# Kernel optimization log

Hardware: AMD Instinct MI355X
Metric: run time of the kernel (lower is better)

Reference implementation:

```python
import jax, jax.numpy as jnp
import numpy as np

N = 100000
E = 1600000
F_IN = 16
HEADS = 4
OUT_CH = 32  # conv_filters[i] // heads = 128 // 4
HID = HEADS * OUT_CH  # 128
N_GRAPHS = 64
N_TARGETS = 4
EPS_BN = 1e-5


def setup_inputs() -> dict:
    key = jax.random.key(0)
    ks = jax.random.split(key, 32)
    glorot = lambda k, shp: jax.random.normal(k, shp, jnp.float32) * np.sqrt(2.0 / (shp[0] + shp[-1]))
    inp = {
        "node_features": jax.random.normal(ks[0], (N, F_IN), jnp.float32),
        "edge_index": jax.random.randint(ks[1], (2, E), 0, N, jnp.int64),
        "batch": jnp.sort(jax.random.randint(ks[2], (N,), 0, N_GRAPHS, jnp.int64)),
        # GAT layer 1: F_IN -> HEADS*OUT_CH
        "W1": glorot(ks[3], (F_IN, HID)),
        "b1": jnp.zeros((HID,), jnp.float32),
        "att_src1": glorot(ks[4], (HEADS, OUT_CH)),
        "att_dst1": glorot(ks[5], (HEADS, OUT_CH)),
        "bn_g1": jnp.ones((HID,), jnp.float32),
        "bn_b1": jnp.zeros((HID,), jnp.float32),
        # GAT layer 2: HID -> HID
        "W2": glorot(ks[6], (HID, HID)),
        "b2": jnp.zeros((HID,), jnp.float32),
        "att_src2": glorot(ks[7], (HEADS, OUT_CH)),
        "att_dst2": glorot(ks[8], (HEADS, OUT_CH)),
        "bn_g2": jnp.ones((HID,), jnp.float32),
        "bn_b2": jnp.zeros((HID,), jnp.float32),
        # dense head 128 -> 64 -> 32 -> 4
        "d1_W": glorot(ks[9], (HID, HID // 2)),
        "d1_b": jnp.zeros((HID // 2,), jnp.float32),
        "bn_g_d1": jnp.ones((HID // 2,), jnp.float32),
        "bn_b_d1": jnp.zeros((HID // 2,), jnp.float32),
        "d2_W": glorot(ks[10], (HID // 2, HID // 4)),
        "d2_b": jnp.zeros((HID // 4,), jnp.float32),
        "bn_g_d2": jnp.ones((HID // 4,), jnp.float32),
        "bn_b_d2": jnp.zeros((HID // 4,), jnp.float32),
        "fc_W": glorot(ks[11], (HID // 4, N_TARGETS)),
        "fc_b": jnp.zeros((N_TARGETS,), jnp.float32),
    }
    return inp


def batch_norm(x, gamma, beta):
    # training-mode BatchNorm1d: biased batch stats over dim 0
    mu = jnp.mean(x, axis=0)
    var = jnp.mean(jnp.square(x - mu), axis=0)
    return gamma * (x - mu) * jax.lax.rsqrt(var + EPS_BN) + beta


def gat_conv(x, src, dst, W, b, att_src, att_dst):
    # PyG GATConv (shared lin, concat heads): h = x @ W -> [N, H, C]
    h = (x @ W).reshape(-1, HEADS, OUT_CH)
    a_s = jnp.sum(h * att_src, axis=-1)  # [N, H]
    a_d = jnp.sum(h * att_dst, axis=-1)  # [N, H]
    e = jax.nn.leaky_relu(a_s[src] + a_d[dst], 0.2)  # [E, H]
    # softmax over incoming edges per destination node
    m = jax.ops.segment_max(e, dst, num_segments=N)
    m = jnp.where(jnp.isfinite(m), m, 0.0)
    w = jnp.exp(e - m[dst])
    s = jax.ops.segment_sum(w, dst, num_segments=N)
    alpha = w / (s[dst] + 1e-16)  # [E, H]
    out = jax.ops.segment_sum(h[src] * alpha[:, :, None], dst, num_segments=N)
    return out.reshape(-1, HID) + b


def reference(node_features, edge_index, batch,
              W1, b1, att_src1, att_dst1, bn_g1, bn_b1,
              W2, b2, att_src2, att_dst2, bn_g2, bn_b2,
              d1_W, d1_b, bn_g_d1, bn_b_d1,
              d2_W, d2_b, bn_g_d2, bn_b_d2,
              fc_W, fc_b):
    src, dst = edge_index[0], edge_index[1]
    x = gat_conv(node_features, src, dst, W1, b1, att_src1, att_dst1)
    x = jax.nn.relu(batch_norm(x, bn_g1, bn_b1))
    x = gat_conv(x, src, dst, W2, b2, att_src2, att_dst2)
    x = jax.nn.relu(batch_norm(x, bn_g2, bn_b2))
    # global mean pool over graphs
    sums = jax.ops.segment_sum(x, batch, num_segments=N_GRAPHS)
    cnt = jax.ops.segment_sum(jnp.ones((x.shape[0],), x.dtype), batch, num_segments=N_GRAPHS)
    g = sums / jnp.maximum(cnt, 1.0)[:, None]  # [G, HID]
    g = jax.nn.relu(batch_norm(g @ d1_W + d1_b, bn_g_d1, bn_b_d1))
    g = jax.nn.relu(batch_norm(g @ d2_W + d2_b, bn_g_d2, bn_b_d2))
    return g @ fc_W + fc_b
```

## Files before the change

kernel.cpp:

```cpp
#include <hip/hip_runtime.h>

#define HID 128
#define NG 64

__device__ __forceinline__ float lrelu(float v) { return v > 0.0f ? v : 0.2f * v; }

__device__ __forceinline__ unsigned int bf16rne(float f) {
    unsigned int u = __float_as_uint(f);
    return (u + 0x7fffu + ((u >> 16) & 1u)) >> 16;
}
__device__ __forceinline__ unsigned int packbf(float a, float b) {
    return bf16rne(a) | (bf16rne(b) << 16);
}

template <int K, bool BN>
__global__ __launch_bounds__(256) void k_gemm(const float* __restrict__ xin,
        const float* __restrict__ W,
        const float* __restrict__ scale, const float* __restrict__ shift,
        const float* __restrict__ attS, const float* __restrict__ attD,
        unsigned short* __restrict__ h, float* __restrict__ as_, float* __restrict__ ad_, int N)
{
    __shared__ float xs[64][K];
    constexpr int K4 = K / 4;
    int t = threadIdx.x;
    int cq = t & 31;
    int nr = t >> 5;

    float4 atS = ((const float4*)attS)[cq];
    float4 atD = ((const float4*)attD)[cq];

    for (int n0 = blockIdx.x * 64; n0 < N; n0 += gridDim.x * 64) {
        int nrem = N - n0; if (nrem > 64) nrem = 64;
        for (int idx = t; idx < 64 * K4; idx += 256) {
            int n = idx / K4, k4 = idx % K4;
            float4 v = make_float4(0.f, 0.f, 0.f, 0.f);
            if (n < nrem) {
                v = ((const float4*)(xin + (size_t)(n0 + n) * K))[k4];
                if (BN) {
                    float4 sc = ((const float4*)scale)[k4];
                    float4 sh = ((const float4*)shift)[k4];
                    v.x = fmaf(v.x, sc.x, sh.x); v.x = v.x > 0.f ? v.x : 0.f;
                    v.y = fmaf(v.y, sc.y, sh.y); v.y = v.y > 0.f ? v.y : 0.f;
                    v.z = fmaf(v.z, sc.z, sh.z); v.z = v.z > 0.f ? v.z : 0.f;
                    v.w = fmaf(v.w, sc.w, sh.w); v.w = v.w > 0.f ? v.w : 0.f;
                }
            }
            *(float4*)(&xs[n][k4 * 4]) = v;
        }
        __syncthreads();

        float4 acc[8];
#pragma unroll
        for (int j = 0; j < 8; ++j) acc[j] = make_float4(0.f, 0.f, 0.f, 0.f);

        const float4* W4 = (const float4*)W;
#pragma unroll 2
        for (int k4 = 0; k4 < K4; ++k4) {
            float4 w0 = W4[(k4 * 4 + 0) * 32 + cq];
            float4 w1 = W4[(k4 * 4 + 1) * 32 + cq];
            float4 w2 = W4[(k4 * 4 + 2) * 32 + cq];
            float4 w3 = W4[(k4 * 4 + 3) * 32 + cq];
#pragma unroll
            for (int j = 0; j < 8; ++j) {
                float4 xv = *(const float4*)(&xs[nr * 8 + j][k4 * 4]);
                acc[j].x = fmaf(xv.x, w0.x, acc[j].x);
                acc[j].y = fmaf(xv.x, w0.y, acc[j].y);
                acc[j].z = fmaf(xv.x, w0.z, acc[j].z);
                acc[j].w = fmaf(xv.x, w0.w, acc[j].w);
                acc[j].x = fmaf(xv.y, w1.x, acc[j].x);
                acc[j].y = fmaf(xv.y, w1.y, acc[j].y);
                acc[j].z = fmaf(xv.y, w1.z, acc[j].z);
                acc[j].w = fmaf(xv.y, w1.w, acc[j].w);
                acc[j].x = fmaf(xv.z, w2.x, acc[j].x);
                acc[j].y = fmaf(xv.z, w2.y, acc[j].y);
                acc[j].z = fmaf(xv.z, w2.z, acc[j].z);
                acc[j].w = fmaf(xv.z, w2.w, acc[j].w);
                acc[j].x = fmaf(xv.w, w3.x, acc[j].x);
                acc[j].y = fmaf(xv.w, w3.y, acc[j].y);
                acc[j].z = fmaf(xv.w, w3.z, acc[j].z);
                acc[j].w = fmaf(xv.w, w3.w, acc[j].w);
            }
        }

#pragma unroll
        for (int j = 0; j < 8; ++j) {
            int n = nr * 8 + j;
            bool ok = (n < nrem);
            if (ok) {
                unsigned int lo = packbf(acc[j].x, acc[j].y);
                unsigned int hi = packbf(acc[j].z, acc[j].w);
                ((uint2*)(h + (size_t)(n0 + n) * 128))[cq] = make_uint2(lo, hi);
            }
            float ps = acc[j].x * atS.x + acc[j].y * atS.y + acc[j].z * atS.z + acc[j].w * atS.w;
            float pd = acc[j].x * atD.x + acc[j].y * atD.y + acc[j].z * atD.z + acc[j].w * atD.w;
            ps += __shfl_xor(ps, 1); pd += __shfl_xor(pd, 1);
            ps += __shfl_xor(ps, 2); pd += __shfl_xor(pd, 2);
            ps += __shfl_xor(ps, 4); pd += __shfl_xor(pd, 4);
            if (ok && (cq & 7) == 0) {
                int hd = cq >> 3;
                as_[(size_t)(n0 + n) * 4 + hd] = ps;
                ad_[(size_t)(n0 + n) * 4 + hd] = pd;
            }
        }
        __syncthreads();
    }
}

__global__ __launch_bounds__(256) void k_bhist(const int* __restrict__ ei,
        int* __restrict__ bSize, int E, int nB)
{
    __shared__ int hist[1024];
    int t = threadIdx.x;
    for (int i = t; i < nB; i += 256) hist[i] = 0;
    __syncthreads();
    int chunk = (E + gridDim.x - 1) / gridDim.x;
    int lo = blockIdx.x * chunk, hi = lo + chunk; if (hi > E) hi = E;
    for (int e = lo + t; e < hi; e += 256) atomicAdd(&hist[ei[E + e] >> 8], 1);
    __syncthreads();
    for (int i = t; i < nB; i += 256) { int c = hist[i]; if (c) atomicAdd(&bSize[i], c); }
}

__global__ __launch_bounds__(512) void k_bscan(const int* __restrict__ bSize,
        int* __restrict__ bOff, int* __restrict__ bCur, int nB)
{
    __shared__ int part[512];
    int t = threadIdx.x;
    part[t] = (t < nB) ? bSize[t] : 0;
    __syncthreads();
    for (int off = 1; off < 512; off <<= 1) {
        int u = (t >= off) ? part[t - off] : 0;
        __syncthreads();
        part[t] += u;
        __syncthreads();
    }
    int ex = (t == 0) ? 0 : part[t - 1];
    if (t < nB) { bOff[t] = ex; bCur[t] = ex; }
    if (t == nB - 1) bOff[nB] = part[t];
}

__global__ __launch_bounds__(256) void k_part(const int* __restrict__ ei,
        int* __restrict__ bCur, unsigned int* __restrict__ bucketBuf, int E, int nB)
{
    __shared__ int hist[1024];
    __shared__ int base[1024];
    int t = threadIdx.x;
    int chunk = (E + gridDim.x - 1) / gridDim.x;
    int lo = blockIdx.x * chunk, hi = lo + chunk; if (hi > E) hi = E;
    for (int i = t; i < nB; i += 256) hist[i] = 0;
    __syncthreads();
    for (int e = lo + t; e < hi; e += 256) atomicAdd(&hist[ei[E + e] >> 8], 1);
    __syncthreads();
    for (int i = t; i < nB; i += 256) {
        int c = hist[i];
        base[i] = c ? atomicAdd(&bCur[i], c) : 0;
        hist[i] = 0;
    }
    __syncthreads();
    for (int e = lo + t; e < hi; e += 256) {
        int s = ei[e], d = ei[E + e];
        int b = d >> 8;
        int pos = base[b] + atomicAdd(&hist[b], 1);
        bucketBuf[pos] = ((unsigned)(d & 255) << 24) | (unsigned)s;
    }
}

__global__ __launch_bounds__(256) void k_build(const unsigned int* __restrict__ bucketBuf,
        const int* __restrict__ bOff, int* __restrict__ rowPtr, int* __restrict__ sSrc, int N)
{
    __shared__ int lhist[256];
    __shared__ int sOut[8192];
    int b = blockIdx.x;
    int dlo = b << 8;
    int dhi = dlo + 256; if (dhi > N) dhi = N;
    int base = bOff[b], end = bOff[b + 1];
    int sz = end - base;
    int t = threadIdx.x;
    lhist[t] = 0;
    __syncthreads();
    for (int i = t; i < sz; i += 256) {
        atomicAdd(&lhist[bucketBuf[base + i] >> 24], 1);
    }
    __syncthreads();
    for (int off = 1; off < 256; off <<= 1) {
        int u = (t >= off) ? lhist[t - off] : 0;
        __syncthreads();
        lhist[t] += u;
        __syncthreads();
    }
    int pfx = (t == 0) ? 0 : lhist[t - 1];
    if (dlo + t < dhi) rowPtr[dlo + t] = base + pfx;
    if (t == 0 && dhi == N) rowPtr[N] = end;
    __syncthreads();
    lhist[t] = pfx;
    __syncthreads();
    if (sz <= 8192) {
        for (int i = t; i < sz; i += 256) {
            unsigned int p = bucketBuf[base + i];
            int pos = atomicAdd(&lhist[p >> 24], 1);
            sOut[pos] = (int)(p & 0xffffffu);
        }
        __syncthreads();
        for (int i = t; i < sz; i += 256) sSrc[base + i] = sOut[i];
    } else {
        for (int i = t; i < sz; i += 256) {
            unsigned int p = bucketBuf[base + i];
            int pos = atomicAdd(&lhist[p >> 24], 1);
            sSrc[base + pos] = (int)(p & 0xffffffu);
        }
    }
}

__global__ __launch_bounds__(256) void k_agg(const int* __restrict__ rowPtr,
        const int* __restrict__ sSrc,
        const float* __restrict__ as_, const float* __restrict__ ad_,
        const unsigned short* __restrict__ h, float* __restrict__ out, int N)
{
    int t = threadIdx.x;
    int lane = t & 31;
    int d = blockIdx.x * 8 + (t >> 5);
    if (d >= N) return;
    int hd = lane >> 3;
    int b0 = rowPtr[d], b1 = rowPtr[d + 1];
    float4 adv = ((const float4*)ad_)[d];

    float4 sm = make_float4(0.f, 0.f, 0.f, 0.f);
    for (int j = b0 + lane; j < b1; j += 32) {
        int s = sSrc[j];
        float4 a = ((const float4*)as_)[s];
        sm.x += __expf(lrelu(a.x + adv.x));
        sm.y += __expf(lrelu(a.y + adv.y));
        sm.z += __expf(lrelu(a.z + adv.z));
        sm.w += __expf(lrelu(a.w + adv.w));
    }
#pragma unroll
    for (int off = 1; off < 32; off <<= 1) {
        sm.x += __shfl_xor(sm.x, off);
        sm.y += __shfl_xor(sm.y, off);
        sm.z += __shfl_xor(sm.z, off);
        sm.w += __shfl_xor(sm.w, off);
    }
    float sumh = (hd == 0) ? sm.x : (hd == 1) ? sm.y : (hd == 2) ? sm.z : sm.w;
    float inv = 1.f / (sumh + 1e-16f);
    float advh = (hd == 0) ? adv.x : (hd == 1) ? adv.y : (hd == 2) ? adv.z : adv.w;

    const uint2* h2 = (const uint2*)h;
    float4 acc = make_float4(0.f, 0.f, 0.f, 0.f);
    int j = b0;
    for (; j + 4 <= b1; j += 4) {
        int s0 = sSrc[j], s1 = sSrc[j + 1], s2 = sSrc[j + 2], s3 = sSrc[j + 3];
        float w0 = __expf(lrelu(as_[(size_t)s0 * 4 + hd] + advh));
        float w1 = __expf(lrelu(as_[(size_t)s1 * 4 + hd] + advh));
        float w2 = __expf(lrelu(as_[(size_t)s2 * 4 + hd] + advh));
        float w3 = __expf(lrelu(as_[(size_t)s3 * 4 + hd] + advh));
        uint2 u0 = h2[(size_t)s0 * 32 + lane];
        uint2 u1 = h2[(size_t)s1 * 32 + lane];
        uint2 u2 = h2[(size_t)s2 * 32 + lane];
        uint2 u3 = h2[(size_t)s3 * 32 + lane];
        acc.x = fmaf(w0, __uint_as_float(u0.x << 16), acc.x);
        acc.y = fmaf(w0, __uint_as_float(u0.x & 0xffff0000u), acc.y);
        acc.z = fmaf(w0, __uint_as_float(u0.y << 16), acc.z);
        acc.w = fmaf(w0, __uint_as_float(u0.y & 0xffff0000u), acc.w);
        acc.x = fmaf(w1, __uint_as_float(u1.x << 16), acc.x);
        acc.y = fmaf(w1, __uint_as_float(u1.x & 0xffff0000u), acc.y);
        acc.z = fmaf(w1, __uint_as_float(u1.y << 16), acc.z);
        acc.w = fmaf(w1, __uint_as_float(u1.y & 0xffff0000u), acc.w);
        acc.x = fmaf(w2, __uint_as_float(u2.x << 16), acc.x);
        acc.y = fmaf(w2, __uint_as_float(u2.x & 0xffff0000u), acc.y);
        acc.z = fmaf(w2, __uint_as_float(u2.y << 16), acc.z);
        acc.w = fmaf(w2, __uint_as_float(u2.y & 0xffff0000u), acc.w);
        acc.x = fmaf(w3, __uint_as_float(u3.x << 16), acc.x);
        acc.y = fmaf(w3, __uint_as_float(u3.x & 0xffff0000u), acc.y);
        acc.z = fmaf(w3, __uint_as_float(u3.y << 16), acc.z);
        acc.w = fmaf(w3, __uint_as_float(u3.y & 0xffff0000u), acc.w);
    }
    for (; j < b1; ++j) {
        int s = sSrc[j];
        float w = __expf(lrelu(as_[(size_t)s * 4 + hd] + advh));
        uint2 u = h2[(size_t)s * 32 + lane];
        acc.x = fmaf(w, __uint_as_float(u.x << 16), acc.x);
        acc.y = fmaf(w, __uint_as_float(u.x & 0xffff0000u), acc.y);
        acc.z = fmaf(w, __uint_as_float(u.y << 16), acc.z);
        acc.w = fmaf(w, __uint_as_float(u.y & 0xffff0000u), acc.w);
    }
    acc.x *= inv; acc.y *= inv; acc.z *= inv; acc.w *= inv;
    ((float4*)out)[(size_t)d * 32 + lane] = acc;
}

__global__ __launch_bounds__(256) void k_bnstats(const float* __restrict__ x,
        double* __restrict__ sums, int N)
{
    __shared__ float r1[256], r2[256];
    int t = threadIdx.x;
    int c = t & 127;
    int half = t >> 7;
    float s1 = 0.f, s2 = 0.f;
    for (int n = blockIdx.x * 2 + half; n < N; n += gridDim.x * 2) {
        float v = x[(size_t)n * 128 + c];
        s1 += v; s2 += v * v;
    }
    r1[t] = s1; r2[t] = s2;
    __syncthreads();
    if (t < 128) {
        s1 = r1[t] + r1[t + 128];
        s2 = r2[t] + r2[t + 128];
        atomicAdd(&sums[t], (double)s1);
        atomicAdd(&sums[128 + t], (double)s2);
    }
}

__global__ __launch_bounds__(128) void k_bnscale(const double* __restrict__ sums,
        const float* __restrict__ gamma, const float* __restrict__ beta,
        float* __restrict__ scale, float* __restrict__ shift, int N)
{
    int c = threadIdx.x;
    double mu = sums[c] / (double)N;
    double var = sums[128 + c] / (double)N - mu * mu;
    if (var < 0.0) var = 0.0;
    double rs = 1.0 / sqrt(var + 1e-5);
    float sc = (float)((double)gamma[c] * rs);
    scale[c] = sc;
    shift[c] = beta[c] - (float)mu * sc;
}

__global__ __launch_bounds__(128) void k_pool(const float* __restrict__ x,
        const int* __restrict__ batch, const float* __restrict__ scale, const float* __restrict__ shift,
        float* __restrict__ gsum, float* __restrict__ gcnt, int N)
{
    int lane = threadIdx.x & 31;
    int r = threadIdx.x >> 5;
    int n0 = blockIdx.x * 64;
    if (n0 >= N) return;
    int n1 = n0 + 64; if (n1 > N) n1 = N;
    float4 sc = ((const float4*)scale)[lane];
    float4 sh = ((const float4*)shift)[lane];
    float4 acc = make_float4(0.f, 0.f, 0.f, 0.f);
    int cnt = 0, cur = -1;
    for (int n = n0 + r; n < n1; n += 4) {
        int g = batch[n];
        if (g != cur) {
            if (cur >= 0) {
                atomicAdd(&gsum[cur * 128 + lane * 4 + 0], acc.x);
                atomicAdd(&gsum[cur * 128 + lane * 4 + 1], acc.y);
                atomicAdd(&gsum[cur * 128 + lane * 4 + 2], acc.z);
                atomicAdd(&gsum[cur * 128 + lane * 4 + 3], acc.w);
                if (lane == 0) atomicAdd(&gcnt[cur], (float)cnt);
            }
            acc = make_float4(0.f, 0.f, 0.f, 0.f); cnt = 0; cur = g;
        }
        float4 v = ((const float4*)x)[(size_t)n * 32 + lane];
        v.x = fmaf(v.x, sc.x, sh.x); v.x = v.x > 0.f ? v.x : 0.f;
        v.y = fmaf(v.y, sc.y, sh.y); v.y = v.y > 0.f ? v.y : 0.f;
        v.z = fmaf(v.z, sc.z, sh.z); v.z = v.z > 0.f ? v.z : 0.f;
        v.w = fmaf(v.w, sc.w, sh.w); v.w = v.w > 0.f ? v.w : 0.f;
        acc.x += v.x; acc.y += v.y; acc.z += v.z; acc.w += v.w;
        cnt++;
    }
    if (cur >= 0) {
        atomicAdd(&gsum[cur * 128 + lane * 4 + 0], acc.x);
        atomicAdd(&gsum[cur * 128 + lane * 4 + 1], acc.y);
        atomicAdd(&gsum[cur * 128 + lane * 4 + 2], acc.z);
        atomicAdd(&gsum[cur * 128 + lane * 4 + 3], acc.w);
        if (lane == 0) atomicAdd(&gcnt[cur], (float)cnt);
    }
}

__global__ __launch_bounds__(256) void k_head(const float* __restrict__ gsum, const float* __restrict__ gcnt,
        const float* __restrict__ d1W, const float* __restrict__ d1b,
        const float* __restrict__ g_d1, const float* __restrict__ b_d1,
        const float* __restrict__ d2W, const float* __restrict__ d2b,
        const float* __restrict__ g_d2, const float* __restrict__ b_d2,
        const float* __restrict__ fcW, const float* __restrict__ fcb,
        float* __restrict__ out)
{
    __shared__ float G[64 * 128];
    __shared__ float Y1[64 * 64];
    __shared__ float Y2[64 * 32];
    int t = threadIdx.x;
    for (int i = t; i < 64 * 128; i += 256) {
        int g = i >> 7;
        float cv = gcnt[g]; if (cv < 1.f) cv = 1.f;
        G[i] = gsum[i] / cv;
    }
    __syncthreads();
    for (int i = t; i < 64 * 64; i += 256) {
        int r = i >> 6, j = i & 63;
        float a = 0.f;
        for (int k = 0; k < 128; ++k) a = fmaf(G[r * 128 + k], d1W[k * 64 + j], a);
        Y1[i] = a + d1b[j];
    }
    __syncthreads();
    if (t < 64) {
        float s1 = 0.f, s2 = 0.f;
        for (int r = 0; r < 64; ++r) { float v = Y1[r * 64 + t]; s1 += v; s2 += v * v; }
        float mu = s1 / 64.f, var = s2 / 64.f - mu * mu; if (var < 0.f) var = 0.f;
        float rs = 1.0f / sqrtf(var + 1e-5f);
        float scv = g_d1[t] * rs, shv = b_d1[t] - mu * scv;
        for (int r = 0; r < 64; ++r) {
            float v = fmaf(Y1[r * 64 + t], scv, shv);
            Y1[r * 64 + t] = v > 0.f ? v : 0.f;
        }
    }
    __syncthreads();
    for (int i = t; i < 64 * 32; i += 256) {
        int r = i >> 5, j = i & 31;
        float a = 0.f;
        for (int k = 0; k < 64; ++k) a = fmaf(Y1[r * 64 + k], d2W[k * 32 + j], a);
        Y2[i] = a + d2b[j];
    }
    __syncthreads();
    if (t < 32) {
        float s1 = 0.f, s2 = 0.f;
        for (int r = 0; r < 64; ++r) { float v = Y2[r * 32 + t]; s1 += v; s2 += v * v; }
        float mu = s1 / 64.f, var = s2 / 64.f - mu * mu; if (var < 0.f) var = 0.f;
        float rs = 1.0f / sqrtf(var + 1e-5f);
        float scv = g_d2[t] * rs, shv = b_d2[t] - mu * scv;
        for (int r = 0; r < 64; ++r) {
            float v = fmaf(Y2[r * 32 + t], scv, shv);
            Y2[r * 32 + t] = v > 0.f ? v : 0.f;
        }
    }
    __syncthreads();
    {
        int r = t >> 2, j = t & 3;
        float a = 0.f;
        for (int k = 0; k < 32; ++k) a = fmaf(Y2[r * 32 + k], fcW[k * 4 + j], a);
        out[t] = a + fcb[j];
    }
}

extern "C" void kernel_launch(void* const* d_in, const int* in_sizes, int n_in,
                              void* d_out, int out_size, void* d_ws, size_t ws_size,
                              hipStream_t stream) {
    const int N = in_sizes[0] / 16;
    const int E = in_sizes[1] / 2;
    const int nB = (N + 255) >> 8;

    const float* x        = (const float*)d_in[0];
    const int*   ei       = (const int*)d_in[1];
    const int*   batch    = (const int*)d_in[2];
    const float* W1       = (const float*)d_in[3];
    const float* att_s1   = (const float*)d_in[5];
    const float* att_d1   = (const float*)d_in[6];
    const float* bn_g1    = (const float*)d_in[7];
    const float* bn_b1    = (const float*)d_in[8];
    const float* W2       = (const float*)d_in[9];
    const float* att_s2   = (const float*)d_in[11];
    const float* att_d2   = (const float*)d_in[12];
    const float* bn_g2    = (const float*)d_in[13];
    const float* bn_b2    = (const float*)d_in[14];
    const float* d1W      = (const float*)d_in[15];
    const float* d1b      = (const float*)d_in[16];
    const float* g_d1     = (const float*)d_in[17];
    const float* b_d1     = (const float*)d_in[18];
    const float* d2W      = (const float*)d_in[19];
    const float* d2b      = (const float*)d_in[20];
    const float* g_d2     = (const float*)d_in[21];
    const float* b_d2     = (const float*)d_in[22];
    const float* fcW      = (const float*)d_in[23];
    const float* fcb      = (const float*)d_in[24];
    float* out = (float*)d_out;

    float* ws = (float*)d_ws;
    size_t o = 0;
    unsigned short* hbuf = (unsigned short*)(ws + o); o += (size_t)N * 64;
    float* outb   = ws + o;  o += (size_t)N * 128;
    float* as_    = ws + o;  o += (size_t)N * 4;
    float* ad_    = ws + o;  o += (size_t)N * 4;
    float* scale1 = ws + o;  o += 128;
    float* shift1 = ws + o;  o += 128;
    float* scale2 = ws + o;  o += 128;
    float* shift2 = ws + o;  o += 128;
    size_t zoff = o;
    double* bnsumA = (double*)(ws + o); o += 512;
    double* bnsumB = (double*)(ws + o); o += 512;
    float* gsum   = ws + o;  o += 64 * 128;
    float* gcnt   = ws + o;  o += 64;
    int*   bSize  = (int*)(ws + o); o += 1024;
    size_t zbytes = (o - zoff) * 4;
    int* rowPtr   = (int*)(ws + o); o += (size_t)N + 1;
    int* sSrc     = (int*)(ws + o); o += E;
    int* bOff     = (int*)(ws + o); o += 1025;
    int* bCur     = (int*)(ws + o); o += 1024;
    unsigned int* bucketBuf = (unsigned int*)(ws + o); o += E;

    hipMemsetAsync(ws + zoff, 0, zbytes, stream);

    k_bhist<<<256, 256, 0, stream>>>(ei, bSize, E, nB);
    k_bscan<<<1, 512, 0, stream>>>(bSize, bOff, bCur, nB);
    k_part<<<256, 256, 0, stream>>>(ei, bCur, bucketBuf, E, nB);
    k_build<<<nB, 256, 0, stream>>>(bucketBuf, bOff, rowPtr, sSrc, N);

    int gemm_grid = (N + 63) / 64;
    int agg_grid = (N + 7) / 8;

    k_gemm<16, false><<<gemm_grid, 256, 0, stream>>>(x, W1, nullptr, nullptr,
            att_s1, att_d1, hbuf, as_, ad_, N);
    k_agg<<<agg_grid, 256, 0, stream>>>(rowPtr, sSrc, as_, ad_, hbuf, outb, N);
    k_bnstats<<<1024, 256, 0, stream>>>(outb, bnsumA, N);
    k_bnscale<<<1, 128, 0, stream>>>(bnsumA, bn_g1, bn_b1, scale1, shift1, N);

    k_gemm<128, true><<<gemm_grid, 256, 0, stream>>>(outb, W2, scale1, shift1,
            att_s2, att_d2, hbuf, as_, ad_, N);
    k_agg<<<agg_grid, 256, 0, stream>>>(rowPtr, sSrc, as_, ad_, hbuf, outb, N);
    k_bnstats<<<1024, 256, 0, stream>>>(outb, bnsumB, N);
    k_bnscale<<<1, 128, 0, stream>>>(bnsumB, bn_g2, bn_b2, scale2, shift2, N);

    k_pool<<<(N + 63) / 64, 128, 0, stream>>>(outb, batch, scale2, shift2, gsum, gcnt, N);
    k_head<<<1, 256, 0, stream>>>(gsum, gcnt, d1W, d1b, g_d1, b_d1,
                                  d2W, d2b, g_d2, b_d2, fcW, fcb, out);
}
```

Measured before the change: 540.8 us.

## Cache attention weights in LDS, fuse BN scale into consumers, vectorize bnstats

The aggregation kernel now stores the per-edge exp attention weights computed in the softmax-sum pass in shared memory (up to 64 edges per node), so the accumulation pass reuses them instead of reloading as_ and recomputing exp. That loop is unrolled by 8 to keep more gathers in flight. The separate BN scale/shift kernels are removed; each gemm and pool block recomputes scale and shift from the double sums into LDS, saving two launches at the cost of redundant per-block work. bnstats is vectorized with float4 loads and runs on fewer blocks.

```diff
diff --git a/kernel.cpp b/kernel.cpp
--- a/kernel.cpp
+++ b/kernel.cpp
@@ -16,15 +16,30 @@
 template <int K, bool BN>
 __global__ __launch_bounds__(256) void k_gemm(const float* __restrict__ xin,
         const float* __restrict__ W,
-        const float* __restrict__ scale, const float* __restrict__ shift,
+        const double* __restrict__ bnsum, const float* __restrict__ gamma, const float* __restrict__ beta,
         const float* __restrict__ attS, const float* __restrict__ attD,
         unsigned short* __restrict__ h, float* __restrict__ as_, float* __restrict__ ad_, int N)
 {
     __shared__ float xs[64][K];
+    __shared__ __align__(16) float sc_s[K];
+    __shared__ __align__(16) float sh_s[K];
     constexpr int K4 = K / 4;
     int t = threadIdx.x;
     int cq = t & 31;
     int nr = t >> 5;
+
+    if (BN) {
+        if (t < K) {
+            double mu = bnsum[t] / (double)N;
+            double var = bnsum[K + t] / (double)N - mu * mu;
+            if (var < 0.0) var = 0.0;
+            double rs = 1.0 / sqrt(var + 1e-5);
+            float sc = (float)((double)gamma[t] * rs);
+            sc_s[t] = sc;
+            sh_s[t] = beta[t] - (float)mu * sc;
+        }
+        __syncthreads();
+    }
 
     float4 atS = ((const float4*)attS)[cq];
     float4 atD = ((const float4*)attD)[cq];
@@ -37,8 +52,8 @@
             if (n < nrem) {
                 v = ((const float4*)(xin + (size_t)(n0 + n) * K))[k4];
                 if (BN) {
-                    float4 sc = ((const float4*)scale)[k4];
-                    float4 sh = ((const float4*)shift)[k4];
+                    float4 sc = ((const float4*)sc_s)[k4];
+                    float4 sh = ((const float4*)sh_s)[k4];
                     v.x = fmaf(v.x, sc.x, sh.x); v.x = v.x > 0.f ? v.x : 0.f;
                     v.y = fmaf(v.y, sc.y, sh.y); v.y = v.y > 0.f ? v.y : 0.f;
                     v.z = fmaf(v.z, sc.z, sh.z); v.z = v.z > 0.f ? v.z : 0.f;
@@ -215,22 +230,27 @@
         const float* __restrict__ as_, const float* __restrict__ ad_,
         const unsigned short* __restrict__ h, float* __restrict__ out, int N)
 {
+    __shared__ float wst[8][64][4];
     int t = threadIdx.x;
     int lane = t & 31;
-    int d = blockIdx.x * 8 + (t >> 5);
-    if (d >= N) return;
-    int hd = lane >> 3;
-    int b0 = rowPtr[d], b1 = rowPtr[d + 1];
-    float4 adv = ((const float4*)ad_)[d];
+    int g = t >> 5;
+    int d = blockIdx.x * 8 + g;
+    bool valid = (d < N);
+    int b0 = 0, deg = 0;
+    float4 adv = make_float4(0.f, 0.f, 0.f, 0.f);
+    if (valid) { b0 = rowPtr[d]; deg = rowPtr[d + 1] - b0; adv = ((const float4*)ad_)[d]; }
 
     float4 sm = make_float4(0.f, 0.f, 0.f, 0.f);
-    for (int j = b0 + lane; j < b1; j += 32) {
-        int s = sSrc[j];
+    for (int e = lane; e < deg; e += 32) {
+        int s = sSrc[b0 + e];
         float4 a = ((const float4*)as_)[s];
-        sm.x += __expf(lrelu(a.x + adv.x));
-        sm.y += __expf(lrelu(a.y + adv.y));
-        sm.z += __expf(lrelu(a.z + adv.z));
-        sm.w += __expf(lrelu(a.w + adv.w));
+        float4 w;
+        w.x = __expf(lrelu(a.x + adv.x));
+        w.y = __expf(lrelu(a.y + adv.y));
+        w.z = __expf(lrelu(a.z + adv.z));
+        w.w = __expf(lrelu(a.w + adv.w));
+        if (e < 64) *(float4*)(&wst[g][e][0]) = w;
+        sm.x += w.x; sm.y += w.y; sm.z += w.z; sm.w += w.w;
     }
 #pragma unroll
     for (int off = 1; off < 32; off <<= 1) {
@@ -239,23 +259,32 @@
         sm.z += __shfl_xor(sm.z, off);
         sm.w += __shfl_xor(sm.w, off);
     }
+    __syncthreads();
+
+    int hd = lane >> 3;
     float sumh = (hd == 0) ? sm.x : (hd == 1) ? sm.y : (hd == 2) ? sm.z : sm.w;
+    float advh = (hd == 0) ? adv.x : (hd == 1) ? adv.y : (hd == 2) ? adv.z : adv.w;
     float inv = 1.f / (sumh + 1e-16f);
-    float advh = (hd == 0) ? adv.x : (hd == 1) ? adv.y : (hd == 2) ? adv.z : adv.w;
 
     const uint2* h2 = (const uint2*)h;
+    const int* sp = sSrc + b0;
     float4 acc = make_float4(0.f, 0.f, 0.f, 0.f);
-    int j = b0;
-    for (; j + 4 <= b1; j += 4) {
-        int s0 = sSrc[j], s1 = sSrc[j + 1], s2 = sSrc[j + 2], s3 = sSrc[j + 3];
-        float w0 = __expf(lrelu(as_[(size_t)s0 * 4 + hd] + advh));
-        float w1 = __expf(lrelu(as_[(size_t)s1 * 4 + hd] + advh));
-        float w2 = __expf(lrelu(as_[(size_t)s2 * 4 + hd] + advh));
-        float w3 = __expf(lrelu(as_[(size_t)s3 * 4 + hd] + advh));
-        uint2 u0 = h2[(size_t)s0 * 32 + lane];
-        uint2 u1 = h2[(size_t)s1 * 32 + lane];
-        uint2 u2 = h2[(size_t)s2 * 32 + lane];
-        uint2 u3 = h2[(size_t)s3 * 32 + lane];
+    int dc = deg < 64 ? deg : 64;
+    int j = 0;
+#define AGG1(S, W) { uint2 u = h2[(size_t)(S) * 32 + lane]; \
+        acc.x = fmaf((W), __uint_as_float(u.x << 16), acc.x); \
+        acc.y = fmaf((W), __uint_as_float(u.x & 0xffff0000u), acc.y); \
+        acc.z = fmaf((W), __uint_as_float(u.y << 16), acc.z); \
+        acc.w = fmaf((W), __uint_as_float(u.y & 0xffff0000u), acc.w); }
+    for (; j + 8 <= dc; j += 8) {
+        int s0 = sp[j], s1 = sp[j+1], s2 = sp[j+2], s3 = sp[j+3];
+        int s4 = sp[j+4], s5 = sp[j+5], s6 = sp[j+6], s7 = sp[j+7];
+        float w0 = wst[g][j][hd],   w1 = wst[g][j+1][hd], w2 = wst[g][j+2][hd], w3 = wst[g][j+3][hd];
+        float w4 = wst[g][j+4][hd], w5 = wst[g][j+5][hd], w6 = wst[g][j+6][hd], w7 = wst[g][j+7][hd];
+        uint2 u0 = h2[(size_t)s0*32+lane], u1 = h2[(size_t)s1*32+lane];
+        uint2 u2 = h2[(size_t)s2*32+lane], u3 = h2[(size_t)s3*32+lane];
+        uint2 u4 = h2[(size_t)s4*32+lane], u5 = h2[(size_t)s5*32+lane];
+        uint2 u6 = h2[(size_t)s6*32+lane], u7 = h2[(size_t)s7*32+lane];
         acc.x = fmaf(w0, __uint_as_float(u0.x << 16), acc.x);
         acc.y = fmaf(w0, __uint_as_float(u0.x & 0xffff0000u), acc.y);
         acc.z = fmaf(w0, __uint_as_float(u0.y << 16), acc.z);
@@ -272,67 +301,100 @@
         acc.y = fmaf(w3, __uint_as_float(u3.x & 0xffff0000u), acc.y);
         acc.z = fmaf(w3, __uint_as_float(u3.y << 16), acc.z);
         acc.w = fmaf(w3, __uint_as_float(u3.y & 0xffff0000u), acc.w);
-    }
-    for (; j < b1; ++j) {
-        int s = sSrc[j];
+        acc.x = fmaf(w4, __uint_as_float(u4.x << 16), acc.x);
+        acc.y = fmaf(w4, __uint_as_float(u4.x & 0xffff0000u), acc.y);
+        acc.z = fmaf(w4, __uint_as_float(u4.y << 16), acc.z);
+        acc.w = fmaf(w4, __uint_as_float(u4.y & 0xffff0000u), acc.w);
+        acc.x = fmaf(w5, __uint_as_float(u5.x << 16), acc.x);
+        acc.y = fmaf(w5, __uint_as_float(u5.x & 0xffff0000u), acc.y);
+        acc.z = fmaf(w5, __uint_as_float(u5.y << 16), acc.z);
+        acc.w = fmaf(w5, __uint_as_float(u5.y & 0xffff0000u), acc.w);
+        acc.x = fmaf(w6, __uint_as_float(u6.x << 16), acc.x);
+        acc.y = fmaf(w6, __uint_as_float(u6.x & 0xffff0000u), acc.y);
+        acc.z = fmaf(w6, __uint_as_float(u6.y << 16), acc.z);
+        acc.w = fmaf(w6, __uint_as_float(u6.y & 0xffff0000u), acc.w);
+        acc.x = fmaf(w7, __uint_as_float(u7.x << 16), acc.x);
+        acc.y = fmaf(w7, __uint_as_float(u7.x & 0xffff0000u), acc.y);
+        acc.z = fmaf(w7, __uint_as_float(u7.y << 16), acc.z);
+        acc.w = fmaf(w7, __uint_as_float(u7.y & 0xffff0000u), acc.w);
+    }
+    for (; j < dc; ++j) {
+        float w = wst[g][j][hd];
+        AGG1(sp[j], w);
+    }
+    for (; j < deg; ++j) {
+        int s = sp[j];
         float w = __expf(lrelu(as_[(size_t)s * 4 + hd] + advh));
-        uint2 u = h2[(size_t)s * 32 + lane];
-        acc.x = fmaf(w, __uint_as_float(u.x << 16), acc.x);
-        acc.y = fmaf(w, __uint_as_float(u.x & 0xffff0000u), acc.y);
-        acc.z = fmaf(w, __uint_as_float(u.y << 16), acc.z);
-        acc.w = fmaf(w, __uint_as_float(u.y & 0xffff0000u), acc.w);
-    }
-    acc.x *= inv; acc.y *= inv; acc.z *= inv; acc.w *= inv;
-    ((float4*)out)[(size_t)d * 32 + lane] = acc;
+        AGG1(s, w);
+    }
+#undef AGG1
+    if (valid) {
+        acc.x *= inv; acc.y *= inv; acc.z *= inv; acc.w *= inv;
+        ((float4*)out)[(size_t)d * 32 + lane] = acc;
+    }
 }
 
 __global__ __launch_bounds__(256) void k_bnstats(const float* __restrict__ x,
         double* __restrict__ sums, int N)
 {
-    __shared__ float r1[256], r2[256];
-    int t = threadIdx.x;
-    int c = t & 127;
-    int half = t >> 7;
-    float s1 = 0.f, s2 = 0.f;
-    for (int n = blockIdx.x * 2 + half; n < N; n += gridDim.x * 2) {
-        float v = x[(size_t)n * 128 + c];
-        s1 += v; s2 += v * v;
+    __shared__ float4 r1[256], r2[256];
+    int t = threadIdx.x;
+    int lane = t & 31;
+    int rg = t >> 5;
+    const float4* x4 = (const float4*)x;
+    float4 s1 = make_float4(0.f, 0.f, 0.f, 0.f);
+    float4 s2 = make_float4(0.f, 0.f, 0.f, 0.f);
+    for (int n = blockIdx.x * 8 + rg; n < N; n += gridDim.x * 8) {
+        float4 v = x4[(size_t)n * 32 + lane];
+        s1.x += v.x; s1.y += v.y; s1.z += v.z; s1.w += v.w;
+        s2.x += v.x * v.x; s2.y += v.y * v.y; s2.z += v.z * v.z; s2.w += v.w * v.w;
     }
     r1[t] = s1; r2[t] = s2;
     __syncthreads();
-    if (t < 128) {
-        s1 = r1[t] + r1[t + 128];
-        s2 = r2[t] + r2[t + 128];
-        atomicAdd(&sums[t], (double)s1);
-        atomicAdd(&sums[128 + t], (double)s2);
-    }
-}
-
-__global__ __launch_bounds__(128) void k_bnscale(const double* __restrict__ sums,
-        const float* __restrict__ gamma, const float* __restrict__ beta,
-        float* __restrict__ scale, float* __restrict__ shift, int N)
-{
-    int c = threadIdx.x;
-    double mu = sums[c] / (double)N;
-    double var = sums[128 + c] / (double)N - mu * mu;
-    if (var < 0.0) var = 0.0;
-    double rs = 1.0 / sqrt(var + 1e-5);
-    float sc = (float)((double)gamma[c] * rs);
-    scale[c] = sc;
-    shift[c] = beta[c] - (float)mu * sc;
+    if (t < 32) {
+        float4 a = r1[t], b = r2[t];
+        for (int k = 1; k < 8; ++k) {
+            float4 c = r1[t + 32 * k], e = r2[t + 32 * k];
+            a.x += c.x; a.y += c.y; a.z += c.z; a.w += c.w;
+            b.x += e.x; b.y += e.y; b.z += e.z; b.w += e.w;
+        }
+        atomicAdd(&sums[t * 4 + 0], (double)a.x);
+        atomicAdd(&sums[t * 4 + 1], (double)a.y);
+        atomicAdd(&sums[t * 4 + 2], (double)a.z);
+        atomicAdd(&sums[t * 4 + 3], (double)a.w);
+        atomicAdd(&sums[128 + t * 4 + 0], (double)b.x);
+        atomicAdd(&sums[128 + t * 4 + 1], (double)b.y);
+        atomicAdd(&sums[128 + t * 4 + 2], (double)b.z);
+        atomicAdd(&sums[128 + t * 4 + 3], (double)b.w);
+    }
 }
 
 __global__ __launch_bounds__(128) void k_pool(const float* __restrict__ x,
-        const int* __restrict__ batch, const float* __restrict__ scale, const float* __restrict__ shift,
+        const int* __restrict__ batch,
+        const double* __restrict__ bnsum, const float* __restrict__ gamma, const float* __restrict__ beta,
         float* __restrict__ gsum, float* __restrict__ gcnt, int N)
 {
-    int lane = threadIdx.x & 31;
-    int r = threadIdx.x >> 5;
+    __shared__ __align__(16) float sc_s[128];
+    __shared__ __align__(16) float sh_s[128];
+    int t = threadIdx.x;
+    {
+        double mu = bnsum[t] / (double)N;
+        double var = bnsum[128 + t] / (double)N - mu * mu;
+        if (var < 0.0) var = 0.0;
+        double rs = 1.0 / sqrt(var + 1e-5);
+        float sc = (float)((double)gamma[t] * rs);
+        sc_s[t] = sc;
+        sh_s[t] = beta[t] - (float)mu * sc;
+    }
+    __syncthreads();
+
+    int lane = t & 31;
+    int r = t >> 5;
     int n0 = blockIdx.x * 64;
     if (n0 >= N) return;
     int n1 = n0 + 64; if (n1 > N) n1 = N;
-    float4 sc = ((const float4*)scale)[lane];
-    float4 sh = ((const float4*)shift)[lane];
+    float4 sc = ((const float4*)sc_s)[lane];
+    float4 sh = ((const float4*)sh_s)[lane];
     float4 acc = make_float4(0.f, 0.f, 0.f, 0.f);
     int cnt = 0, cur = -1;
     for (int n = n0 + r; n < n1; n += 4) {
@@ -466,10 +528,6 @@
     float* outb   = ws + o;  o += (size_t)N * 128;
     float* as_    = ws + o;  o += (size_t)N * 4;
     float* ad_    = ws + o;  o += (size_t)N * 4;
-    float* scale1 = ws + o;  o += 128;
-    float* shift1 = ws + o;  o += 128;
-    float* scale2 = ws + o;  o += 128;
-    float* shift2 = ws + o;  o += 128;
     size_t zoff = o;
     double* bnsumA = (double*)(ws + o); o += 512;
     double* bnsumB = (double*)(ws + o); o += 512;
@@ -493,19 +551,17 @@
     int gemm_grid = (N + 63) / 64;
     int agg_grid = (N + 7) / 8;
 
-    k_gemm<16, false><<<gemm_grid, 256, 0, stream>>>(x, W1, nullptr, nullptr,
+    k_gemm<16, false><<<gemm_grid, 256, 0, stream>>>(x, W1, nullptr, nullptr, nullptr,
             att_s1, att_d1, hbuf, as_, ad_, N);
     k_agg<<<agg_grid, 256, 0, stream>>>(rowPtr, sSrc, as_, ad_, hbuf, outb, N);
-    k_bnstats<<<1024, 256, 0, stream>>>(outb, bnsumA, N);
-    k_bnscale<<<1, 128, 0, stream>>>(bnsumA, bn_g1, bn_b1, scale1, shift1, N);
-
-    k_gemm<128, true><<<gemm_grid, 256, 0, stream>>>(outb, W2, scale1, shift1,
+    k_bnstats<<<512, 256, 0, stream>>>(outb, bnsumA, N);
+
+    k_gemm<128, true><<<gemm_grid, 256, 0, stream>>>(outb, W2, bnsumA, bn_g1, bn_b1,
             att_s2, att_d2, hbuf, as_, ad_, N);
     k_agg<<<agg_grid, 256, 0, stream>>>(rowPtr, sSrc, as_, ad_, hbuf, outb, N);
-    k_bnstats<<<1024, 256, 0, stream>>>(outb, bnsumB, N);
-    k_bnscale<<<1, 128, 0, stream>>>(bnsumB, bn_g2, bn_b2, scale2, shift2, N);
-
-    k_pool<<<(N + 63) / 64, 128, 0, stream>>>(outb, batch, scale2, shift2, gsum, gcnt, N);
+    k_bnstats<<<512, 256, 0, stream>>>(outb, bnsumB, N);
+
+    k_pool<<<(N + 63) / 64, 128, 0, stream>>>(outb, batch, bnsumB, bn_g2, bn_b2, gsum, gcnt, N);
     k_head<<<1, 256, 0, stream>>>(gsum, gcnt, d1W, d1b, g_d1, b_d1,
                                   d2W, d2b, g_d2, b_d2, fcW, fcb, out);
 }
```

Result: slower. 605.8 us (+12.0%).
